# Kernel tuning notes

Hardware: AMD Instinct MI355X
Metric: run time of the kernel (lower is better)

The kernel has to match this reference:

```python
import jax, jax.numpy as jnp
import numpy as np


def _dwconv(x, w, pad, dil=1):
    # x: [B,C,H,W], w: [C,1,kh,kw] depthwise
    C = x.shape[1]
    return jax.lax.conv_general_dilated(
        x, w, window_strides=(1, 1), padding=[(pad, pad), (pad, pad)],
        rhs_dilation=(dil, dil),
        dimension_numbers=('NCHW', 'OIHW', 'NCHW'),
        feature_group_count=C)


def _conv1x1(x, w, b):
    # w: [O,C,1,1]
    return jnp.einsum('bchw,oc->bohw', x, w[:, :, 0, 0]) + b[None, :, None, None]


def _ln(x, g, b, eps=1e-6):
    mu = x.mean(-1, keepdims=True)
    var = ((x - mu) ** 2).mean(-1, keepdims=True)
    return (x - mu) * jax.lax.rsqrt(var + eps) * g + b


def _gelu(x):
    return jax.nn.gelu(x, approximate=False)  # torch nn.GELU default = exact erf


def _starts(h, step, ps):
    s = []
    for i in range(0, h + step - ps, step):
        s.append(i if i + ps <= h else h - ps)
    return np.asarray(s, np.int32)


def _divisor(h, w, step, ps):
    # replicates patch_reverse's overlap /2 strips exactly
    div = np.ones((h, w), np.float32)
    for i in range(step, h + step - ps, step):
        top, down = i, i + ps - step
        if top + ps > h:
            top = h - ps
        div[top:down, :] *= 2.0
    for j in range(step, w + step - ps, step):
        left, right = j, j + ps - step
        if left + ps > w:
            left = w - ps
        div[:, left:right] *= 2.0
    return div


def _forward(x, ps, lth_dw_w, lth_pw_w, lth_pw_b, lth_gate_w, lth_gate_b, lth_scale,
             ln1_g, ln1_b, ln2_g, ln2_b, qkv_w, gate_w, gate_b, proj_w, pe_w, pe_b,
             fc1_w, fc1_b, dw_w, dw_b, fc2_w, fc2_b):
    B, C, H, W = x.shape
    step = ps - 2
    # ---- Low_to_high ----
    low = x.reshape(B, C, H // 2, 2, W // 2, 2).mean(axis=(3, 5))  # adaptive avg pool (even H,W)
    low_up = jax.image.resize(low, (B, C, H, W), method='bilinear')  # align_corners=False
    hf = x - low_up
    sgate = jax.nn.sigmoid(_conv1x1(jnp.abs(hf), lth_gate_w, lth_gate_b))  # [B,1,H,W]
    refined = _conv1x1(_gelu(_dwconv(hf, lth_dw_w, pad=2, dil=2)), lth_pw_w, lth_pw_b)
    x = x + lth_scale * refined * sgate
    # ---- patch_divide (overlapping windows) ----
    st = ps if (H == ps and W == ps) else step
    tops, lefts = _starts(H, st, ps), _starts(W, st, ps)
    nh, nw = len(tops), len(lefts)
    r = tops[:, None] + np.arange(ps)   # [nh, ps]
    c = lefts[:, None] + np.arange(ps)  # [nw, ps]
    crop = x[:, :, r[:, None, :, None], c[None, :, None, :]]  # [B,C,nh,nw,ps,ps]
    t = crop.transpose(0, 2, 3, 4, 5, 1).reshape(B * nh * nw, ps * ps, C)  # (b n) (h w) c
    # ---- Attention (single-head, qk_dim == dim) ----
    y = _ln(t, ln1_g, ln1_b)
    qkv = y @ qkv_w                      # [Bn, N, 3C]
    q, k, v = jnp.split(qkv, 3, axis=-1)
    z = _gelu(y @ gate_w + gate_b)       # gate
    qimg = q.transpose(0, 2, 1).reshape(-1, C, ps, ps)
    pe = (_dwconv(qimg, pe_w, pad=1) + pe_b[None, :, None, None])
    pe = pe.reshape(-1, C, ps * ps).transpose(0, 2, 1)
    scale = C ** (-0.5)                  # qk_dim = dim = C
    attn = jax.nn.softmax(jnp.einsum('bnc,bmc->bnm', q, k) * scale, axis=-1)
    out = jnp.einsum('bnm,bmc->bnc', attn, v) + pe
    t = (out * z) @ proj_w + t           # proj + residual
    # ---- patch_reverse (overlap-add, strips averaged) ----
    crop = t.reshape(B, nh, nw, ps, ps, C).transpose(0, 5, 1, 2, 3, 4)  # [B,C,nh,nw,ps,ps]
    summed = jnp.zeros_like(x).at[:, :, r[:, None, :, None], c[None, :, None, :]].add(crop)
    x = summed * (1.0 / jnp.asarray(_divisor(H, W, st, ps)))
    # ---- ConvFFN ----
    xt = x.reshape(B, C, H * W).transpose(0, 2, 1)  # [B,HW,C]
    y = _ln(xt, ln2_g, ln2_b)
    y = _gelu(y @ fc1_w + fc1_b)                    # [B,HW,2C]
    yimg = y.transpose(0, 2, 1).reshape(B, -1, H, W)
    y = y + (_dwconv(yimg, dw_w, pad=2) + dw_b[None, :, None, None]).reshape(B, -1, H * W).transpose(0, 2, 1)
    y = y @ fc2_w + fc2_b
    xt = y + xt
    return xt.transpose(0, 2, 1).reshape(B, C, H, W)


def setup_inputs() -> dict:
    key = jax.random.key(0)
    ks = jax.random.split(key, 16)
    B, C, H, W = 8, 128, 128, 128
    HID = 2 * C
    def w(i, shape, s=0.02):
        return jax.random.normal(ks[i], shape, jnp.float32) * s
    return {
        'x': jax.random.normal(ks[0], (B, C, H, W), jnp.float32),
        'ps': 16,
        'lth_dw_w': w(1, (C, 1, 3, 3), 0.1),
        'lth_pw_w': w(2, (C, C, 1, 1)),
        'lth_pw_b': jnp.zeros((C,), jnp.float32),
        'lth_gate_w': w(3, (1, C, 1, 1), 0.1),
        'lth_gate_b': jnp.zeros((1,), jnp.float32),
        'lth_scale': w(4, (1, C, 1, 1), 0.1),
        'ln1_g': jnp.ones((C,), jnp.float32),
        'ln1_b': jnp.zeros((C,), jnp.float32),
        'ln2_g': jnp.ones((C,), jnp.float32),
        'ln2_b': jnp.zeros((C,), jnp.float32),
        'qkv_w': w(5, (C, 3 * C)),
        'gate_w': w(6, (C, C)),
        'gate_b': jnp.zeros((C,), jnp.float32),
        'proj_w': w(7, (C, C)),
        'pe_w': w(8, (C, 1, 3, 3), 0.1),
        'pe_b': jnp.zeros((C,), jnp.float32),
        'fc1_w': w(9, (C, HID)),
        'fc1_b': jnp.zeros((HID,), jnp.float32),
        'dw_w': w(10, (HID, 1, 5, 5), 0.1),
        'dw_b': jnp.zeros((HID,), jnp.float32),
        'fc2_w': w(11, (HID, C)),
        'fc2_b': jnp.zeros((C,), jnp.float32),
    }


def reference(x, ps, lth_dw_w, lth_pw_w, lth_pw_b, lth_gate_w, lth_gate_b, lth_scale,
              ln1_g, ln1_b, ln2_g, ln2_b, qkv_w, gate_w, gate_b, proj_w, pe_w, pe_b,
              fc1_w, fc1_b, dw_w, dw_b, fc2_w, fc2_b):
    return _forward(x, ps, lth_dw_w, lth_pw_w, lth_pw_b, lth_gate_w, lth_gate_b, lth_scale,
                    ln1_g, ln1_b, ln2_g, ln2_b, qkv_w, gate_w, gate_b, proj_w, pe_w, pe_b,
                    fc1_w, fc1_b, dw_w, dw_b, fc2_w, fc2_b)
```

## Files before the change

### kernel.cpp

```cpp
#include <hip/hip_runtime.h>
#include <hip/hip_bf16.h>
#include <math.h>

typedef __hip_bfloat16 bf16;
typedef __attribute__((ext_vector_type(8))) short bf16x8;
typedef __attribute__((ext_vector_type(4))) float f32x4;

static constexpr int B_ = 8, C_ = 128, H_ = 128, W_ = 128;
static constexpr int N_ = H_ * W_;
static constexpr int NWIN = 648;

__device__ __forceinline__ float b2f(bf16 v) { return __bfloat162float(v); }
__device__ __forceinline__ bf16 f2b(float v) { return __float2bfloat16(v); }

__device__ __forceinline__ float gelu_f(float x) {
    float xs = x * 0.70710678118654752f;
    float ax = fabsf(xs);
    float t = 1.0f / fmaf(0.3275911f, ax, 1.0f);
    float poly = t * fmaf(t, fmaf(t, fmaf(t, fmaf(t, 1.061405429f, -1.453152027f), 1.421413741f), -0.284496736f), 0.254829592f);
    float erf_ax = fmaf(-poly, __expf(-ax * ax), 1.0f);
    float erfv = copysignf(erf_ax, xs);
    return 0.5f * x * (1.0f + erfv);
}

__device__ __forceinline__ void load_row12(const char* tile, int a, int wg, float* dst) {
    int base = a * 288 + wg * 16;
    union { uint4 u; bf16 hh[8]; } c0, c1, c2;
    c0.u = *(const uint4*)(tile + base);
    c1.u = *(const uint4*)(tile + base + 16);
    c2.u = *(const uint4*)(tile + base + 32);
    dst[0] = b2f(c0.hh[6]); dst[1] = b2f(c0.hh[7]);
    #pragma unroll
    for (int j = 0; j < 8; ++j) dst[2 + j] = b2f(c1.hh[j]);
    dst[10] = b2f(c2.hh[0]); dst[11] = b2f(c2.hh[1]);
}

__global__ __launch_bounds__(256) void k_wprep(const float* __restrict__ projw, const float* __restrict__ qkvw,
                                               const float* __restrict__ gatew, const float* __restrict__ w1,
                                               const float* __restrict__ w2, const float* __restrict__ pww,
                                               bf16* __restrict__ wt, bf16* __restrict__ wqkv,
                                               bf16* __restrict__ wt1, bf16* __restrict__ wt2,
                                               bf16* __restrict__ wpw) {
    int idx = blockIdx.x * 256 + threadIdx.x;
    if (idx < 16384) {
        int o = idx >> 7, c = idx & 127;
        wt[idx] = f2b(projw[c * 128 + o]);
    } else if (idx < 81920) {
        int i = idx - 16384; int o = i >> 7, c = i & 127;
        wqkv[i] = f2b((o < 384) ? qkvw[c * 384 + o] : gatew[c * 128 + (o - 384)]);
    } else if (idx < 114688) {
        int i = idx - 81920; int o = i >> 7, c = i & 127;
        wt1[i] = f2b(w1[c * 256 + o]);
    } else if (idx < 147456) {
        int i = idx - 114688; int o = i >> 8, c = i & 255;
        wt2[i] = f2b(w2[c * 128 + o]);
    } else {
        int i = idx - 147456;
        wpw[i] = f2b(pww[i]);
    }
}

__global__ __launch_bounds__(256) void k_hf2(const float* __restrict__ x, bf16* __restrict__ hf) {
    __shared__ float lowt[10][64];
    int tid = threadIdx.x;
    int bid = blockIdx.x;
    int ht = bid & 7, c = (bid >> 3) & 127, b = bid >> 10;
    const float* xp = x + (size_t)(b * C_ + c) * N_;
    int h0 = ht * 16;
    int lo0 = (h0 >> 1) - 1;
    for (int e = tid; e < 640; e += 256) {
        int lr = e >> 6, jc = e & 63;
        int j = lo0 + lr; j = j < 0 ? 0 : (j > 63 ? 63 : j);
        const float* pr = xp + (2 * j) * W_ + 2 * jc;
        lowt[lr][jc] = (pr[0] + pr[1] + pr[W_] + pr[W_ + 1]) * 0.25f;
    }
    __syncthreads();
    int hl = tid >> 4, wg = tid & 15;
    int h = h0 + hl;
    int jh = h >> 1;
    int j0, j1; float wh0, wh1;
    if (h & 1) { j0 = jh; j1 = jh + 1 > 63 ? 63 : jh + 1; wh0 = 0.75f; wh1 = 0.25f; }
    else       { j0 = jh - 1 < 0 ? 0 : jh - 1; j1 = jh;   wh0 = 0.25f; wh1 = 0.75f; }
    int l0 = j0 - lo0, l1 = j1 - lo0;
    float4 xa = *(const float4*)(xp + h * W_ + wg * 8);
    float4 xb = *(const float4*)(xp + h * W_ + wg * 8 + 4);
    float xv[8] = {xa.x, xa.y, xa.z, xa.w, xb.x, xb.y, xb.z, xb.w};
    union { bf16 hh[8]; uint4 u; } outv;
    #pragma unroll
    for (int k2 = 0; k2 < 8; ++k2) {
        int w = wg * 8 + k2;
        int jw = w >> 1;
        int w0, w1; float ww0, ww1;
        if (w & 1) { w0 = jw; w1 = jw + 1 > 63 ? 63 : jw + 1; ww0 = 0.75f; ww1 = 0.25f; }
        else       { w0 = jw - 1 < 0 ? 0 : jw - 1; w1 = jw;   ww0 = 0.25f; ww1 = 0.75f; }
        float up = wh0 * (ww0 * lowt[l0][w0] + ww1 * lowt[l0][w1])
                 + wh1 * (ww0 * lowt[l1][w0] + ww1 * lowt[l1][w1]);
        outv.hh[k2] = f2b(xv[k2] - up);
    }
    *(uint4*)(hf + (size_t)(b * C_ + c) * N_ + h * W_ + wg * 8) = outv.u;
}

__global__ __launch_bounds__(256) void k_sgate(const bf16* __restrict__ hf, const float* __restrict__ gw,
                                               const float* __restrict__ gb, float* __restrict__ sg) {
    int idx = blockIdx.x * 256 + threadIdx.x;
    int n = idx & (N_ - 1); int b = idx >> 14;
    const bf16* p = hf + (size_t)b * C_ * N_ + n;
    float s = 0.f;
    for (int c = 0; c < C_; ++c) s += gw[c] * fabsf(b2f(p[(size_t)c * N_]));
    s += gb[0];
    sg[idx] = 1.0f / (1.0f + __expf(-s));
}

__global__ __launch_bounds__(256) void k_dw3p(const bf16* __restrict__ hf, const float* __restrict__ wdw,
                                              bf16* __restrict__ g) {
    __shared__ __align__(16) char tile[38016];
    int tid = threadIdx.x;
    int bid = blockIdx.x;
    int ch = bid & 127, b = bid >> 7;
    const bf16* p = hf + (size_t)(b * C_ + ch) * N_;
    for (int e = tid; e < 2376; e += 256) *(uint4*)(tile + e * 16) = (uint4){0, 0, 0, 0};
    __syncthreads();
    for (int e = tid; e < 2048; e += 256) {
        int gr = e >> 4, slot = e & 15;
        uint4 val = *(const uint4*)(p + gr * 128 + slot * 8);
        *(uint4*)(tile + (gr + 2) * 288 + 16 + slot * 16) = val;
    }
    float kw[9];
    #pragma unroll
    for (int j = 0; j < 9; ++j) kw[j] = wdw[ch * 9 + j];
    __syncthreads();
    int hg = tid >> 4, wg = tid & 15;
    int h0 = hg * 8;
    float ring[5][12];
    #pragma unroll
    for (int j = 0; j < 4; ++j) load_row12(tile, h0 + j, wg, ring[j]);
    bf16* op = g + (size_t)(b * C_ + ch) * N_;
    #pragma unroll
    for (int rr = 0; rr < 8; ++rr) {
        load_row12(tile, h0 + rr + 4, wg, ring[(rr + 4) % 5]);
        float acc[8] = {};
        #pragma unroll
        for (int ky = 0; ky < 3; ++ky) {
            const float* e = ring[(rr + 2 * ky) % 5];
            #pragma unroll
            for (int ow = 0; ow < 8; ++ow) {
                acc[ow] = fmaf(kw[ky * 3 + 0], e[ow], acc[ow]);
                acc[ow] = fmaf(kw[ky * 3 + 1], e[ow + 2], acc[ow]);
                acc[ow] = fmaf(kw[ky * 3 + 2], e[ow + 4], acc[ow]);
            }
        }
        union { bf16 h[8]; uint4 u; } outv;
        #pragma unroll
        for (int ow = 0; ow < 8; ++ow) outv.h[ow] = f2b(gelu_f(acc[ow]));
        *(uint4*)(op + (h0 + rr) * 128 + wg * 8) = outv.u;
    }
}

__global__ __launch_bounds__(256) void k_pw_mfma(const bf16* __restrict__ g, const bf16* __restrict__ wpw,
                                                 const float* __restrict__ pwb, const float* __restrict__ x,
                                                 const float* __restrict__ scale, const float* __restrict__ sg,
                                                 bf16* __restrict__ x1) {
    __shared__ __align__(16) char lds[49152];
    int tid = threadIdx.x;
    int lane = tid & 63, w = tid >> 6;
    int l15 = lane & 15, lhi = lane >> 4;
    int gtok = blockIdx.x * 64; int b = gtok >> 14; int nb = gtok & (N_ - 1);
    char* wch = lds + 16384;
    for (int e = tid; e < 8192; e += 256) {
        int c = e >> 6, i = e & 63;
        bf16 val = g[(size_t)(b * C_ + c) * N_ + nb + i];
        *(bf16*)(lds + i * 256 + ((2 * c) ^ ((i & 7) << 4))) = val;
    }
    for (int e = tid; e < 2048; e += 256) {
        int row = e >> 4, slot = e & 15;
        uint4 val = *(const uint4*)((const char*)wpw + row * 256 + slot * 16);
        *(uint4*)(wch + row * 256 + ((slot * 16) ^ ((row & 7) << 4))) = val;
    }
    __syncthreads();
    bf16x8 afr[4];
    {
        int row = w * 16 + l15;
        #pragma unroll
        for (int cc = 0; cc < 4; ++cc) {
            int cbyt = cc * 64 + lhi * 16;
            afr[cc] = *(const bf16x8*)(lds + row * 256 + (cbyt ^ ((row & 7) << 4)));
        }
    }
    f32x4 acc[8];
    #pragma unroll
    for (int t = 0; t < 8; ++t) acc[t] = (f32x4){0.f, 0.f, 0.f, 0.f};
    #pragma unroll
    for (int ot = 0; ot < 8; ++ot) {
        int row = ot * 16 + l15;
        #pragma unroll
        for (int cc = 0; cc < 4; ++cc) {
            int cbyt = cc * 64 + lhi * 16;
            bf16x8 bfr = *(const bf16x8*)(wch + row * 256 + (cbyt ^ ((row & 7) << 4)));
            acc[ot] = __builtin_amdgcn_mfma_f32_16x16x32_bf16(afr[cc], bfr, acc[ot], 0, 0, 0);
        }
    }
    int n0 = nb + w * 16 + lhi * 4;
    float4 sg4 = *(const float4*)&sg[b * N_ + n0];
    #pragma unroll
    for (int ot = 0; ot < 8; ++ot) {
        int o = ot * 16 + l15;
        size_t obase = (size_t)(b * C_ + o) * N_ + n0;
        float4 x4 = *(const float4*)&x[obase];
        float sc = scale[o], bi = pwb[o];
        union { bf16 h[4]; uint2 u; } t4;
        t4.h[0] = f2b(x4.x + sc * (acc[ot][0] + bi) * sg4.x);
        t4.h[1] = f2b(x4.y + sc * (acc[ot][1] + bi) * sg4.y);
        t4.h[2] = f2b(x4.z + sc * (acc[ot][2] + bi) * sg4.z);
        t4.h[3] = f2b(x4.w + sc * (acc[ot][3] + bi) * sg4.w);
        *(uint2*)(x1 + obase) = t4.u;
    }
}

__global__ __launch_bounds__(256) void k_qkv_mfma(const bf16* __restrict__ x1, const float* __restrict__ lng,
                                                  const float* __restrict__ lnb, const bf16* __restrict__ wall,
                                                  const float* __restrict__ gateb,
                                                  bf16* __restrict__ q, bf16* __restrict__ k,
                                                  bf16* __restrict__ v, bf16* __restrict__ z) {
    __shared__ __align__(16) char lds[49664];
    __shared__ float red2[8][64];
    __shared__ float mu_l[64], rs_l[64];
    int tid = threadIdx.x;
    int lane = tid & 63, w = tid >> 6;
    int l15 = lane & 15, lhi = lane >> 4;
    int win = blockIdx.x >> 2; int qbase = (blockIdx.x & 3) * 64;
    int b = win / 81; int r0 = win % 81; int top = (r0 / 9) * 14, left = (r0 % 9) * 14;
    float* xf = (float*)(lds + 16384);
    char* wchunk = lds + 16384;
    for (int e = tid; e < 8192; e += 256) {
        int c = e >> 6, i = e & 63; int tok = qbase + i; int p = tok >> 4, qq = tok & 15;
        xf[c * 65 + i] = b2f(x1[(size_t)(b * C_ + c) * N_ + (top + p) * W_ + (left + qq)]);
    }
    __syncthreads();
    {
        int i = tid & 63, r = tid >> 6;
        float s = 0.f, ss = 0.f;
        for (int cc = r * 32; cc < r * 32 + 32; ++cc) { float vv = xf[cc * 65 + i]; s += vv; ss += vv * vv; }
        red2[r][i] = s; red2[4 + r][i] = ss;
    }
    __syncthreads();
    if (tid < 64) {
        float s = red2[0][tid] + red2[1][tid] + red2[2][tid] + red2[3][tid];
        float ss = red2[4][tid] + red2[5][tid] + red2[6][tid] + red2[7][tid];
        float mu = s * (1.f / 128.f); float var = ss * (1.f / 128.f) - mu * mu;
        mu_l[tid] = mu; rs_l[tid] = rsqrtf(var + 1e-6f);
    }
    __syncthreads();
    {
        int c = tid & 127;
        float g = lng[c], be = lnb[c];
        for (int e = tid; e < 8192; e += 256) {
            int i = e >> 7;
            float val = (xf[c * 65 + i] - mu_l[i]) * rs_l[i] * g + be;
            *(bf16*)(lds + i * 256 + ((2 * c) ^ ((i & 7) << 4))) = f2b(val);
        }
    }
    __syncthreads();
    bf16x8 afr[4];
    {
        int row = w * 16 + l15;
        #pragma unroll
        for (int cc = 0; cc < 4; ++cc) {
            int cbyt = cc * 64 + lhi * 16;
            afr[cc] = *(const bf16x8*)(lds + row * 256 + (cbyt ^ ((row & 7) << 4)));
        }
    }
    for (int pass = 0; pass < 4; ++pass) {
        __syncthreads();
        for (int e = tid; e < 2048; e += 256) {
            int row = e >> 4, slot = e & 15;
            uint4 val = *(const uint4*)((const char*)wall + (size_t)(pass * 128 + row) * 256 + slot * 16);
            *(uint4*)(wchunk + row * 256 + ((slot * 16) ^ ((row & 7) << 4))) = val;
        }
        __syncthreads();
        f32x4 acc[8];
        #pragma unroll
        for (int t = 0; t < 8; ++t) acc[t] = (f32x4){0.f, 0.f, 0.f, 0.f};
        #pragma unroll
        for (int ot = 0; ot < 8; ++ot) {
            int row = ot * 16 + l15;
            #pragma unroll
            for (int cc = 0; cc < 4; ++cc) {
                int cbyt = cc * 64 + lhi * 16;
                bf16x8 bfr = *(const bf16x8*)(wchunk + row * 256 + (cbyt ^ ((row & 7) << 4)));
                acc[ot] = __builtin_amdgcn_mfma_f32_16x16x32_bf16(afr[cc], bfr, acc[ot], 0, 0, 0);
            }
        }
        if (pass != 2) {
            bf16* outp = (pass == 0) ? q : (pass == 1) ? k : z;
            bool gel = (pass == 3);
            #pragma unroll
            for (int ot = 0; ot < 8; ++ot) {
                int o = ot * 16 + l15;
                float gb = gel ? gateb[o] : 0.f;
                #pragma unroll
                for (int r = 0; r < 4; ++r) {
                    int gtok = qbase + w * 16 + lhi * 4 + r;
                    float vv = acc[ot][r];
                    outp[((size_t)win * 256 + gtok) * 128 + o] = gel ? f2b(gelu_f(vv + gb)) : f2b(vv);
                }
            }
        } else {
            #pragma unroll
            for (int ot = 0; ot < 8; ++ot) {
                int o = ot * 16 + l15;
                union { bf16 h[4]; uint2 u; } t4;
                #pragma unroll
                for (int r = 0; r < 4; ++r) t4.h[r] = f2b(acc[ot][r]);
                *(uint2*)(v + (size_t)win * 32768 + (size_t)o * 256 + qbase + w * 16 + lhi * 4) = t4.u;
            }
        }
    }
}

__global__ __launch_bounds__(256) void k_attn_mfma(const bf16* __restrict__ qb, const bf16* __restrict__ kb,
                                                   const bf16* __restrict__ vb, bf16* __restrict__ ob) {
    __shared__ __align__(16) char lds[49152];
    int tid = threadIdx.x;
    int lane = tid & 63, w = tid >> 6;
    int l15 = lane & 15, lhi = lane >> 4;
    int xcd = blockIdx.x & 7, ixd = blockIdx.x >> 3;
    int win = xcd * 81 + (ixd >> 2);
    int qbase = (ixd & 3) * 64;
    const bf16* qg = qb + ((size_t)win * 256 + qbase) * 128;
    const bf16* kg = kb + (size_t)win * 256 * 128;
    const bf16* vg = vb + (size_t)win * 128 * 256;
    char* chunk = lds + 32768;
    for (int e = tid; e < 1024; e += 256) {
        int row = e >> 4, slot = e & 15;
        uint4 val = *(const uint4*)((const char*)qg + row * 256 + slot * 16);
        *(uint4*)(lds + row * 256 + ((slot * 16) ^ ((row & 7) << 4))) = val;
    }
    __syncthreads();
    bf16x8 afr[4];
    {
        int row = w * 16 + l15;
        #pragma unroll
        for (int cc = 0; cc < 4; ++cc) {
            int cb = cc * 64 + lhi * 16;
            afr[cc] = *(const bf16x8*)(lds + row * 256 + (cb ^ ((row & 7) << 4)));
        }
    }
    f32x4 acc[16];
    #pragma unroll
    for (int t = 0; t < 16; ++t) acc[t] = (f32x4){0.f, 0.f, 0.f, 0.f};
    for (int kc = 0; kc < 4; ++kc) {
        __syncthreads();
        for (int e = tid; e < 1024; e += 256) {
            int row = e >> 4, slot = e & 15;
            uint4 val = *(const uint4*)((const char*)kg + (size_t)(kc * 64 + row) * 256 + slot * 16);
            *(uint4*)(chunk + row * 256 + ((slot * 16) ^ ((row & 7) << 4))) = val;
        }
        __syncthreads();
        #pragma unroll
        for (int t = 0; t < 4; ++t) {
            int row = t * 16 + l15;
            #pragma unroll
            for (int cc = 0; cc < 4; ++cc) {
                int cb = cc * 64 + lhi * 16;
                bf16x8 bfr = *(const bf16x8*)(chunk + row * 256 + (cb ^ ((row & 7) << 4)));
                acc[kc * 4 + t] = __builtin_amdgcn_mfma_f32_16x16x32_bf16(afr[cc], bfr, acc[kc * 4 + t], 0, 0, 0);
            }
        }
    }
    const float sm_scale = 0.08838834764831845f;
    #pragma unroll
    for (int r = 0; r < 4; ++r) {
        float m = -1e30f;
        #pragma unroll
        for (int t = 0; t < 16; ++t) m = fmaxf(m, acc[t][r]);
        #pragma unroll
        for (int d2 = 1; d2 < 16; d2 <<= 1) m = fmaxf(m, __shfl_xor(m, d2, 64));
        float ssum = 0.f;
        #pragma unroll
        for (int t = 0; t < 16; ++t) { float p = __expf((acc[t][r] - m) * sm_scale); acc[t][r] = p; ssum += p; }
        #pragma unroll
        for (int d2 = 1; d2 < 16; d2 <<= 1) ssum += __shfl_xor(ssum, d2, 64);
        float inv = 1.f / ssum;
        #pragma unroll
        for (int t = 0; t < 16; ++t) acc[t][r] *= inv;
    }
    #pragma unroll
    for (int t = 0; t < 16; ++t) {
        #pragma unroll
        for (int r = 0; r < 4; ++r) {
            int row = w * 16 + lhi * 4 + r;
            int cb = (t * 16 + l15) * 2;
            *(bf16*)(lds + row * 512 + (cb ^ ((row & 7) << 4))) = f2b(acc[t][r]);
        }
    }
    f32x4 oacc[8];
    #pragma unroll
    for (int t = 0; t < 8; ++t) oacc[t] = (f32x4){0.f, 0.f, 0.f, 0.f};
    for (int vc = 0; vc < 4; ++vc) {
        __syncthreads();
        for (int e = tid; e < 1024; e += 256) {
            int row = e >> 3, slot = e & 7;
            uint4 val = *(const uint4*)((const char*)vg + (size_t)row * 512 + vc * 128 + slot * 16);
            *(uint4*)(chunk + row * 128 + ((slot * 16) ^ ((row & 7) << 4))) = val;
        }
        __syncthreads();
        #pragma unroll
        for (int jc = 0; jc < 2; ++jc) {
            int prow = w * 16 + l15;
            int pcb = vc * 128 + jc * 64 + lhi * 16;
            bf16x8 ap = *(const bf16x8*)(lds + prow * 512 + (pcb ^ ((prow & 7) << 4)));
            #pragma unroll
            for (int ct = 0; ct < 8; ++ct) {
                int vrow = ct * 16 + l15;
                int vcb = jc * 64 + lhi * 16;
                bf16x8 bv = *(const bf16x8*)(chunk + vrow * 128 + (vcb ^ ((vrow & 7) << 4)));
                oacc[ct] = __builtin_amdgcn_mfma_f32_16x16x32_bf16(bv, ap, oacc[ct], 0, 0, 0);
            }
        }
    }
    bf16* og = ob + ((size_t)win * 256 + qbase) * 128;
    {
        int tok = w * 16 + l15;
        #pragma unroll
        for (int ct = 0; ct < 8; ++ct) {
            int c4 = ct * 16 + lhi * 4;
            union { bf16 h[4]; uint2 u; } t4;
            #pragma unroll
            for (int r = 0; r < 4; ++r) t4.h[r] = f2b(oacc[ct][r]);
            *(uint2*)(og + tok * 128 + c4) = t4.u;
        }
    }
}

__global__ __launch_bounds__(256) void k_peg(bf16* __restrict__ ob, const bf16* __restrict__ qb,
                                             const bf16* __restrict__ zb,
                                             const float* __restrict__ pew, const float* __restrict__ peb) {
    __shared__ float pw_lds[1152];
    __shared__ float pb_lds[128];
    int tid = threadIdx.x;
    for (int e = tid; e < 1152; e += 256) pw_lds[e] = pew[e];
    if (tid < 128) pb_lds[tid] = peb[tid];
    __syncthreads();
    int g = blockIdx.x * 256 + tid;
    int c8 = g & 15, tok = (g >> 4) & 255, win = g >> 12;
    int cb = c8 * 8;
    int pp = tok >> 4, qq = tok & 15;
    size_t base = ((size_t)win * 256 + tok) * 128 + cb;
    float pv[8];
    #pragma unroll
    for (int cc = 0; cc < 8; ++cc) pv[cc] = pb_lds[cb + cc];
    #pragma unroll
    for (int ky = 0; ky < 3; ++ky) {
        int py = pp + ky - 1; if ((unsigned)py >= 16u) continue;
        #pragma unroll
        for (int kx = 0; kx < 3; ++kx) {
            int qx = qq + kx - 1; if ((unsigned)qx >= 16u) continue;
            union { uint4 u; bf16 h[8]; } qu;
            qu.u = *(const uint4*)(qb + ((size_t)win * 256 + py * 16 + qx) * 128 + cb);
            #pragma unroll
            for (int cc = 0; cc < 8; ++cc)
                pv[cc] += pw_lds[(cb + cc) * 9 + ky * 3 + kx] * b2f(qu.h[cc]);
        }
    }
    union { uint4 u; bf16 h[8]; } ou, zu, ru;
    ou.u = *(const uint4*)(ob + base);
    zu.u = *(const uint4*)(zb + base);
    #pragma unroll
    for (int cc = 0; cc < 8; ++cc)
        ru.h[cc] = f2b((b2f(ou.h[cc]) + pv[cc]) * b2f(zu.h[cc]));
    *(uint4*)(ob + base) = ru.u;
}

__global__ __launch_bounds__(256) void k_proj(const bf16* __restrict__ ub, const bf16* __restrict__ wt,
                                              const bf16* __restrict__ x1, bf16* __restrict__ t2) {
    __shared__ __align__(16) char lds[49152];
    int tid = threadIdx.x;
    int lane = tid & 63, w = tid >> 6;
    int l15 = lane & 15, lhi = lane >> 4;
    int win = blockIdx.x >> 2, qbase = (blockIdx.x & 3) * 64;
    int b = win / 81; int r0 = win % 81; int top = (r0 / 9) * 14, left = (r0 % 9) * 14;
    const bf16* ug = ub + ((size_t)win * 256 + qbase) * 128;
    char* wchunk = lds + 16384;
    for (int e = tid; e < 1024; e += 256) {
        int row = e >> 4, slot = e & 15;
        uint4 val = *(const uint4*)((const char*)ug + row * 256 + slot * 16);
        *(uint4*)(lds + row * 256 + ((slot * 16) ^ ((row & 7) << 4))) = val;
    }
    for (int e = tid; e < 2048; e += 256) {
        int row = e >> 4, slot = e & 15;
        uint4 val = *(const uint4*)((const char*)wt + row * 256 + slot * 16);
        *(uint4*)(wchunk + row * 256 + ((slot * 16) ^ ((row & 7) << 4))) = val;
    }
    __syncthreads();
    bf16x8 afr[4];
    {
        int row = w * 16 + l15;
        #pragma unroll
        for (int cc = 0; cc < 4; ++cc) {
            int cbyt = cc * 64 + lhi * 16;
            afr[cc] = *(const bf16x8*)(lds + row * 256 + (cbyt ^ ((row & 7) << 4)));
        }
    }
    f32x4 acc[8];
    #pragma unroll
    for (int t = 0; t < 8; ++t) acc[t] = (f32x4){0.f, 0.f, 0.f, 0.f};
    #pragma unroll
    for (int ot = 0; ot < 8; ++ot) {
        int row = ot * 16 + l15;
        #pragma unroll
        for (int cc = 0; cc < 4; ++cc) {
            int cbyt = cc * 64 + lhi * 16;
            bf16x8 bfr = *(const bf16x8*)(wchunk + row * 256 + (cbyt ^ ((row & 7) << 4)));
            acc[ot] = __builtin_amdgcn_mfma_f32_16x16x32_bf16(afr[cc], bfr, acc[ot], 0, 0, 0);
        }
    }
    int gtok0 = qbase + w * 16 + lhi * 4;
    int p = gtok0 >> 4, qq = gtok0 & 15;
    #pragma unroll
    for (int ot = 0; ot < 8; ++ot) {
        int o = ot * 16 + l15;
        const uint* xr32 = (const uint*)(x1 + (size_t)(b * C_ + o) * N_ + (top + p) * W_ + left + qq);
        union { uint u2[2]; bf16 h[4]; } xv;
        xv.u2[0] = xr32[0]; xv.u2[1] = xr32[1];
        union { bf16 h[4]; uint2 u; } t4;
        #pragma unroll
        for (int r = 0; r < 4; ++r) t4.h[r] = f2b(acc[ot][r] + b2f(xv.h[r]));
        *(uint2*)(t2 + (size_t)win * 32768 + (size_t)o * 256 + gtok0) = t4.u;
    }
}

__global__ __launch_bounds__(256) void k_fc1ln(const bf16* __restrict__ t2, const float* __restrict__ lng,
                                               const float* __restrict__ lnb, const bf16* __restrict__ wt1,
                                               const float* __restrict__ b1, bf16* __restrict__ h1,
                                               bf16* __restrict__ x2w) {
    __shared__ __align__(16) char lds[49664];
    __shared__ float red2[8][64];
    __shared__ float mu_l[64], rs_l[64];
    int tid = threadIdx.x;
    int lane = tid & 63, w = tid >> 6;
    int l15 = lane & 15, lhi = lane >> 4;
    int gtok = blockIdx.x * 64; int b = gtok >> 14; int nb = gtok & (N_ - 1);
    int h = nb >> 7, w0 = nb & 127;
    int imin = (h < 16) ? 0 : (h - 2) / 14; int imax = h / 14; if (imax > 8) imax = 8;
    int jmin0 = (w0 < 16) ? 0 : (w0 - 2) / 14;
    int jmax0 = (w0 + 63) / 14; if (jmax0 > 8) jmax0 = 8;
    float* xf = (float*)(lds + 16384);
    char* wch = lds + 16384;
    for (int e = tid; e < 8320; e += 256) xf[e] = 0.f;
    __syncthreads();
    {
        int c = tid >> 1, half = tid & 1;
        for (int ii = imin; ii <= imax; ++ii) {
            int trow = h - ii * 14;
            for (int jj = jmin0; jj <= jmax0; ++jj) {
                int s = jj * 14 - w0 + half * 8;
                if (s >= 0 && s <= 56) {
                    const bf16* tp = t2 + (size_t)((b * 9 + ii) * 9 + jj) * 32768
                                   + (size_t)c * 256 + trow * 16 + half * 8;
                    union { uint4 u; bf16 hh[8]; } qv;
                    qv.u = *(const uint4*)tp;
                    float* xr = xf + c * 65 + s;
                    #pragma unroll
                    for (int k2 = 0; k2 < 8; ++k2) xr[k2] += b2f(qv.hh[k2]);
                }
            }
        }
    }
    __syncthreads();
    for (int e = tid; e < 2048; e += 256) {
        int c = e >> 4, qd = e & 15;
        int i0 = qd * 4;
        union { bf16 hh[4]; uint2 u; } t4;
        #pragma unroll
        for (int k2 = 0; k2 < 4; ++k2) {
            int i = i0 + k2;
            int wp = w0 + i;
            int jmn = (wp < 16) ? 0 : (wp - 2) / 14; int jmx = wp / 14; if (jmx > 8) jmx = 8;
            float inv = 1.0f / (float)((imax - imin + 1) * (jmx - jmn + 1));
            float val = xf[c * 65 + i] * inv;
            xf[c * 65 + i] = val;
            t4.hh[k2] = f2b(val);
        }
        *(uint2*)(x2w + (size_t)(b * C_ + c) * N_ + nb + i0) = t4.u;
    }
    __syncthreads();
    {
        int i = tid & 63, r = tid >> 6;
        float s = 0.f, ss = 0.f;
        for (int cc = r * 32; cc < r * 32 + 32; ++cc) { float vv = xf[cc * 65 + i]; s += vv; ss += vv * vv; }
        red2[r][i] = s; red2[4 + r][i] = ss;
    }
    __syncthreads();
    if (tid < 64) {
        float s = red2[0][tid] + red2[1][tid] + red2[2][tid] + red2[3][tid];
        float ss = red2[4][tid] + red2[5][tid] + red2[6][tid] + red2[7][tid];
        float mu = s * (1.f / 128.f); float var = ss * (1.f / 128.f) - mu * mu;
        mu_l[tid] = mu; rs_l[tid] = rsqrtf(var + 1e-6f);
    }
    __syncthreads();
    {
        int c = tid & 127;
        float g = lng[c], be = lnb[c];
        for (int e = tid; e < 8192; e += 256) {
            int i = e >> 7;
            float val = (xf[c * 65 + i] - mu_l[i]) * rs_l[i] * g + be;
            *(bf16*)(lds + i * 256 + ((2 * c) ^ ((i & 7) << 4))) = f2b(val);
        }
    }
    __syncthreads();
    bf16x8 afr[4];
    {
        int row = w * 16 + l15;
        #pragma unroll
        for (int cc = 0; cc < 4; ++cc) {
            int cbyt = cc * 64 + lhi * 16;
            afr[cc] = *(const bf16x8*)(lds + row * 256 + (cbyt ^ ((row & 7) << 4)));
        }
    }
    for (int p = 0; p < 2; ++p) {
        __syncthreads();
        for (int e = tid; e < 2048; e += 256) {
            int row = e >> 4, slot = e & 15;
            uint4 val = *(const uint4*)((const char*)wt1 + (size_t)(p * 128 + row) * 256 + slot * 16);
            *(uint4*)(wch + row * 256 + ((slot * 16) ^ ((row & 7) << 4))) = val;
        }
        __syncthreads();
        f32x4 acc[8];
        #pragma unroll
        for (int t = 0; t < 8; ++t) acc[t] = (f32x4){0.f, 0.f, 0.f, 0.f};
        #pragma unroll
        for (int ot = 0; ot < 8; ++ot) {
            int row = ot * 16 + l15;
            #pragma unroll
            for (int cc = 0; cc < 4; ++cc) {
                int cbyt = cc * 64 + lhi * 16;
                bf16x8 bfr = *(const bf16x8*)(wch + row * 256 + (cbyt ^ ((row & 7) << 4)));
                acc[ot] = __builtin_amdgcn_mfma_f32_16x16x32_bf16(afr[cc], bfr, acc[ot], 0, 0, 0);
            }
        }
        int n0 = nb + w * 16 + lhi * 4;
        #pragma unroll
        for (int ot = 0; ot < 8; ++ot) {
            int o = p * 128 + ot * 16 + l15;
            float bi = b1[o];
            union { bf16 h[4]; uint2 u; } t4;
            #pragma unroll
            for (int r = 0; r < 4; ++r) t4.h[r] = f2b(gelu_f(acc[ot][r] + bi));
            *(uint2*)(h1 + (size_t)(b * 256 + o) * N_ + n0) = t4.u;
        }
    }
}

__global__ __launch_bounds__(256) void k_dw5p(const bf16* __restrict__ h1, const float* __restrict__ wdw,
                                              const float* __restrict__ bdw, bf16* __restrict__ h2) {
    __shared__ __align__(16) char tile[38016];
    int tid = threadIdx.x;
    int bid = blockIdx.x;
    int ch = bid & 255, b = bid >> 8;
    const bf16* p = h1 + (size_t)(b * 256 + ch) * N_;
    for (int e = tid; e < 2376; e += 256) *(uint4*)(tile + e * 16) = (uint4){0, 0, 0, 0};
    __syncthreads();
    for (int e = tid; e < 2048; e += 256) {
        int gr = e >> 4, slot = e & 15;
        uint4 val = *(const uint4*)(p + gr * 128 + slot * 8);
        *(uint4*)(tile + (gr + 2) * 288 + 16 + slot * 16) = val;
    }
    float kw[25];
    #pragma unroll
    for (int j = 0; j < 25; ++j) kw[j] = wdw[ch * 25 + j];
    float bi = bdw[ch];
    __syncthreads();
    int hg = tid >> 4, wg = tid & 15;
    int h0 = hg * 8;
    float ring[5][12];
    #pragma unroll
    for (int j = 0; j < 4; ++j) load_row12(tile, h0 + j, wg, ring[j]);
    bf16* op = h2 + (size_t)(b * 256 + ch) * N_;
    #pragma unroll
    for (int rr = 0; rr < 8; ++rr) {
        load_row12(tile, h0 + rr + 4, wg, ring[(rr + 4) % 5]);
        float acc[8];
        #pragma unroll
        for (int ow = 0; ow < 8; ++ow) acc[ow] = bi;
        #pragma unroll
        for (int ky = 0; ky < 5; ++ky) {
            const float* e = ring[(rr + ky) % 5];
            #pragma unroll
            for (int ow = 0; ow < 8; ++ow) {
                #pragma unroll
                for (int kx = 0; kx < 5; ++kx)
                    acc[ow] = fmaf(kw[ky * 5 + kx], e[ow + kx], acc[ow]);
            }
        }
        {
            const float* e = ring[(rr + 2) % 5];
            #pragma unroll
            for (int ow = 0; ow < 8; ++ow) acc[ow] += e[ow + 2];
        }
        union { bf16 h[8]; uint4 u; } outv;
        #pragma unroll
        for (int ow = 0; ow < 8; ++ow) outv.h[ow] = f2b(acc[ow]);
        *(uint4*)(op + (h0 + rr) * 128 + wg * 8) = outv.u;
    }
}

__global__ __launch_bounds__(256) void k_fc2_mfma(const bf16* __restrict__ h2, const bf16* __restrict__ wt2,
                                                  const float* __restrict__ b2, const bf16* __restrict__ x2,
                                                  float* __restrict__ out) {
    __shared__ __align__(16) char lds[65536];
    int tid = threadIdx.x;
    int lane = tid & 63, w = tid >> 6;
    int l15 = lane & 15, lhi = lane >> 4;
    int gtok = blockIdx.x * 64; int b = gtok >> 14; int nb = gtok & (N_ - 1);
    char* wch = lds + 32768;
    for (int e = tid; e < 16384; e += 256) {
        int c = e >> 6, i = e & 63;
        bf16 val = h2[(size_t)(b * 256 + c) * N_ + nb + i];
        *(bf16*)(lds + i * 512 + ((2 * c) ^ ((i & 7) << 4))) = val;
    }
    __syncthreads();
    bf16x8 afr[8];
    {
        int row = w * 16 + l15;
        #pragma unroll
        for (int cc = 0; cc < 8; ++cc) {
            int cbyt = cc * 64 + lhi * 16;
            afr[cc] = *(const bf16x8*)(lds + row * 512 + (cbyt ^ ((row & 7) << 4)));
        }
    }
    f32x4 acc[8];
    #pragma unroll
    for (int t = 0; t < 8; ++t) acc[t] = (f32x4){0.f, 0.f, 0.f, 0.f};
    for (int kh = 0; kh < 2; ++kh) {
        __syncthreads();
        for (int e = tid; e < 2048; e += 256) {
            int row = e >> 4, slot = e & 15;
            uint4 val = *(const uint4*)((const char*)wt2 + (size_t)row * 512 + kh * 256 + slot * 16);
            *(uint4*)(wch + row * 256 + ((slot * 16) ^ ((row & 7) << 4))) = val;
        }
        __syncthreads();
        #pragma unroll
        for (int ot = 0; ot < 8; ++ot) {
            int row = ot * 16 + l15;
            #pragma unroll
            for (int cc = 0; cc < 4; ++cc) {
                int cbyt = cc * 64 + lhi * 16;
                bf16x8 bfr = *(const bf16x8*)(wch + row * 256 + (cbyt ^ ((row & 7) << 4)));
                acc[ot] = __builtin_amdgcn_mfma_f32_16x16x32_bf16(afr[kh * 4 + cc], bfr, acc[ot], 0, 0, 0);
            }
        }
    }
    int n0 = nb + w * 16 + lhi * 4;
    #pragma unroll
    for (int ot = 0; ot < 8; ++ot) {
        int o = ot * 16 + l15;
        size_t obase = (size_t)(b * C_ + o) * N_ + n0;
        float bi = b2[o];
        union { uint2 u; bf16 h[4]; } xr;
        xr.u = *(const uint2*)(x2 + obase);
        float4 r4;
        r4.x = acc[ot][0] + bi + b2f(xr.h[0]);
        r4.y = acc[ot][1] + bi + b2f(xr.h[1]);
        r4.z = acc[ot][2] + bi + b2f(xr.h[2]);
        r4.w = acc[ot][3] + bi + b2f(xr.h[3]);
        *(float4*)(out + obase) = r4;
    }
}

extern "C" void kernel_launch(void* const* d_in, const int* in_sizes, int n_in,
                              void* d_out, int out_size, void* d_ws, size_t ws_size,
                              hipStream_t stream) {
    const float* x         = (const float*)d_in[0];
    const float* lth_dw_w  = (const float*)d_in[2];
    const float* lth_pw_w  = (const float*)d_in[3];
    const float* lth_pw_b  = (const float*)d_in[4];
    const float* lth_gate_w= (const float*)d_in[5];
    const float* lth_gate_b= (const float*)d_in[6];
    const float* lth_scale = (const float*)d_in[7];
    const float* ln1_g     = (const float*)d_in[8];
    const float* ln1_b     = (const float*)d_in[9];
    const float* ln2_g     = (const float*)d_in[10];
    const float* ln2_b     = (const float*)d_in[11];
    const float* qkv_w     = (const float*)d_in[12];
    const float* gate_w    = (const float*)d_in[13];
    const float* gate_b    = (const float*)d_in[14];
    const float* proj_w    = (const float*)d_in[15];
    const float* pe_w      = (const float*)d_in[16];
    const float* pe_b      = (const float*)d_in[17];
    const float* fc1_w     = (const float*)d_in[18];
    const float* fc1_b     = (const float*)d_in[19];
    const float* dw_w      = (const float*)d_in[20];
    const float* dw_b      = (const float*)d_in[21];
    const float* fc2_w     = (const float*)d_in[22];
    const float* fc2_b     = (const float*)d_in[23];

    char* ws = (char*)d_ws;
    constexpr size_t SZ_X = 33554432;
    constexpr size_t SZ_W = 42467328;
    constexpr size_t OFF_A = 0;
    constexpr size_t OFF_B = OFF_A + SZ_X;
    constexpr size_t OFF_C = OFF_B + SZ_W;
    constexpr size_t OFF_D = OFF_C + SZ_W;
    constexpr size_t OFF_E = OFF_D + SZ_W;
    constexpr size_t OFF_F = OFF_E + SZ_W;
    constexpr size_t OFF_G = OFF_F + SZ_W;
    constexpr size_t OFF_H = OFF_G + 32768;
    constexpr size_t OFF_I = OFF_H + 131072;

    bf16*  x1  = (bf16*)(ws + OFF_A);
    bf16*  h2  = (bf16*)(ws + OFF_A);
    float* sg  = (float*)(ws + OFF_B + 16777216);
    bf16*  o   = (bf16*)(ws + OFF_B);
    bf16*  q   = (bf16*)(ws + OFF_C);
    bf16*  x2  = (bf16*)(ws + OFF_C);
    bf16*  hf  = (bf16*)(ws + OFF_D);
    bf16*  k   = (bf16*)(ws + OFF_D);
    bf16*  t2  = (bf16*)(ws + OFF_D);
    bf16*  g   = (bf16*)(ws + OFF_E);
    bf16*  v   = (bf16*)(ws + OFF_E);
    bf16*  h1  = (bf16*)(ws + OFF_E);
    bf16*  z   = (bf16*)(ws + OFF_F);
    bf16*  wt  = (bf16*)(ws + OFF_G);
    bf16*  wqkv= (bf16*)(ws + OFF_H);
    bf16*  wt1 = (bf16*)(ws + OFF_I);
    bf16*  wt2 = (bf16*)(ws + OFF_I + 65536);
    bf16*  wpw = (bf16*)(ws + OFF_I + 131072);

    k_wprep   <<<640,   256, 0, stream>>>(proj_w, qkv_w, gate_w, fc1_w, fc2_w, lth_pw_w,
                                          wt, wqkv, wt1, wt2, wpw);
    k_hf2     <<<8192,  256, 0, stream>>>(x, hf);
    k_sgate   <<<512,   256, 0, stream>>>(hf, lth_gate_w, lth_gate_b, sg);
    k_dw3p    <<<1024,  256, 0, stream>>>(hf, lth_dw_w, g);
    k_pw_mfma <<<2048,  256, 0, stream>>>(g, wpw, lth_pw_b, x, lth_scale, sg, x1);
    k_qkv_mfma<<<2592,  256, 0, stream>>>(x1, ln1_g, ln1_b, wqkv, gate_b, q, k, v, z);
    k_attn_mfma<<<2592, 256, 0, stream>>>(q, k, v, o);
    k_peg     <<<10368, 256, 0, stream>>>(o, q, z, pe_w, pe_b);
    k_proj    <<<2592,  256, 0, stream>>>(o, wt, x1, t2);
    k_fc1ln   <<<2048,  256, 0, stream>>>(t2, ln2_g, ln2_b, wt1, fc1_b, h1, x2);
    k_dw5p    <<<2048,  256, 0, stream>>>(h1, dw_w, dw_b, h2);
    k_fc2_mfma<<<2048,  256, 0, stream>>>(h2, wt2, fc2_b, x2, (float*)d_out);
}
```

Baseline: 509.0 us.

## Software-pipeline K and V tile loads through registers in attention kernel

```diff
diff --git a/kernel.cpp b/kernel.cpp
--- a/kernel.cpp
+++ b/kernel.cpp
@@ -329,12 +329,25 @@
     const bf16* qg = qb + ((size_t)win * 256 + qbase) * 128;
     const bf16* kg = kb + (size_t)win * 256 * 128;
     const bf16* vg = vb + (size_t)win * 128 * 256;
+    char* kbuf0 = lds + 16384;
+    char* kbuf1 = lds + 32768;
     char* chunk = lds + 32768;
+    uint4 sreg[4];
     for (int e = tid; e < 1024; e += 256) {
         int row = e >> 4, slot = e & 15;
         uint4 val = *(const uint4*)((const char*)qg + row * 256 + slot * 16);
         *(uint4*)(lds + row * 256 + ((slot * 16) ^ ((row & 7) << 4))) = val;
     }
+    #pragma unroll
+    for (int j = 0; j < 4; ++j) {
+        int e = tid + j * 256; int row = e >> 4, slot = e & 15;
+        sreg[j] = *(const uint4*)((const char*)kg + (size_t)row * 256 + slot * 16);
+    }
+    #pragma unroll
+    for (int j = 0; j < 4; ++j) {
+        int e = tid + j * 256; int row = e >> 4, slot = e & 15;
+        *(uint4*)(kbuf0 + row * 256 + ((slot * 16) ^ ((row & 7) << 4))) = sreg[j];
+    }
     __syncthreads();
     bf16x8 afr[4];
     {
@@ -348,24 +361,35 @@
     f32x4 acc[16];
     #pragma unroll
     for (int t = 0; t < 16; ++t) acc[t] = (f32x4){0.f, 0.f, 0.f, 0.f};
+    #pragma unroll
     for (int kc = 0; kc < 4; ++kc) {
-        __syncthreads();
-        for (int e = tid; e < 1024; e += 256) {
-            int row = e >> 4, slot = e & 15;
-            uint4 val = *(const uint4*)((const char*)kg + (size_t)(kc * 64 + row) * 256 + slot * 16);
-            *(uint4*)(chunk + row * 256 + ((slot * 16) ^ ((row & 7) << 4))) = val;
-        }
-        __syncthreads();
+        if (kc < 3) {
+            #pragma unroll
+            for (int j = 0; j < 4; ++j) {
+                int e = tid + j * 256; int row = e >> 4, slot = e & 15;
+                sreg[j] = *(const uint4*)((const char*)kg + (size_t)((kc + 1) * 64 + row) * 256 + slot * 16);
+            }
+        }
+        char* buf = (kc & 1) ? kbuf1 : kbuf0;
         #pragma unroll
         for (int t = 0; t < 4; ++t) {
             int row = t * 16 + l15;
             #pragma unroll
             for (int cc = 0; cc < 4; ++cc) {
                 int cb = cc * 64 + lhi * 16;
-                bf16x8 bfr = *(const bf16x8*)(chunk + row * 256 + (cb ^ ((row & 7) << 4)));
+                bf16x8 bfr = *(const bf16x8*)(buf + row * 256 + (cb ^ ((row & 7) << 4)));
                 acc[kc * 4 + t] = __builtin_amdgcn_mfma_f32_16x16x32_bf16(afr[cc], bfr, acc[kc * 4 + t], 0, 0, 0);
             }
         }
+        if (kc < 3) {
+            char* dbuf = (kc & 1) ? kbuf0 : kbuf1;
+            #pragma unroll
+            for (int j = 0; j < 4; ++j) {
+                int e = tid + j * 256; int row = e >> 4, slot = e & 15;
+                *(uint4*)(dbuf + row * 256 + ((slot * 16) ^ ((row & 7) << 4))) = sreg[j];
+            }
+        }
+        __syncthreads();
     }
     const float sm_scale = 0.08838834764831845f;
     #pragma unroll
@@ -383,6 +407,11 @@
         float inv = 1.f / ssum;
         #pragma unroll
         for (int t = 0; t < 16; ++t) acc[t][r] *= inv;
+    }
+    #pragma unroll
+    for (int j = 0; j < 4; ++j) {
+        int e = tid + j * 256; int row = e >> 3, slot = e & 7;
+        sreg[j] = *(const uint4*)((const char*)vg + (size_t)row * 512 + slot * 16);
     }
     #pragma unroll
     for (int t = 0; t < 16; ++t) {
@@ -393,17 +422,24 @@
             *(bf16*)(lds + row * 512 + (cb ^ ((row & 7) << 4))) = f2b(acc[t][r]);
         }
     }
+    #pragma unroll
+    for (int j = 0; j < 4; ++j) {
+        int e = tid + j * 256; int row = e >> 3, slot = e & 7;
+        *(uint4*)(chunk + row * 128 + ((slot * 16) ^ ((row & 7) << 4))) = sreg[j];
+    }
+    __syncthreads();
     f32x4 oacc[8];
     #pragma unroll
     for (int t = 0; t < 8; ++t) oacc[t] = (f32x4){0.f, 0.f, 0.f, 0.f};
+    #pragma unroll
     for (int vc = 0; vc < 4; ++vc) {
-        __syncthreads();
-        for (int e = tid; e < 1024; e += 256) {
-            int row = e >> 3, slot = e & 7;
-            uint4 val = *(const uint4*)((const char*)vg + (size_t)row * 512 + vc * 128 + slot * 16);
-            *(uint4*)(chunk + row * 128 + ((slot * 16) ^ ((row & 7) << 4))) = val;
-        }
-        __syncthreads();
+        if (vc < 3) {
+            #pragma unroll
+            for (int j = 0; j < 4; ++j) {
+                int e = tid + j * 256; int row = e >> 3, slot = e & 7;
+                sreg[j] = *(const uint4*)((const char*)vg + (size_t)row * 512 + (vc + 1) * 128 + slot * 16);
+            }
+        }
         #pragma unroll
         for (int jc = 0; jc < 2; ++jc) {
             int prow = w * 16 + l15;
@@ -416,6 +452,15 @@
                 bf16x8 bv = *(const bf16x8*)(chunk + vrow * 128 + (vcb ^ ((vrow & 7) << 4)));
                 oacc[ct] = __builtin_amdgcn_mfma_f32_16x16x32_bf16(bv, ap, oacc[ct], 0, 0, 0);
             }
+        }
+        if (vc < 3) {
+            __syncthreads();
+            #pragma unroll
+            for (int j = 0; j < 4; ++j) {
+                int e = tid + j * 256; int row = e >> 3, slot = e & 7;
+                *(uint4*)(chunk + row * 128 + ((slot * 16) ^ ((row & 7) << 4))) = sreg[j];
+            }
+            __syncthreads();
         }
     }
     bf16* og = ob + ((size_t)win * 256 + qbase) * 128;
```

Result: slower. 565.2 us (+11.0%).
